# Kernel optimization log

Measured on AMD Instinct MI355X. Metric: run time of the kernel, lower is better.

Reference implementation:

```python
import jax, jax.numpy as jnp
import numpy as np

B, CIN, COUT, H, W, K, PAD, STRIDE = 32, 64, 64, 224, 224, 3, 1, 1


def setup_inputs() -> dict:
    key = jax.random.key(0)
    kx, kw, kb = jax.random.split(key, 3)
    x = jax.random.normal(kx, (B, CIN, H, W), dtype=jnp.float32)
    weight = jax.random.normal(kw, (COUT, CIN, K, K), dtype=jnp.float32)
    bias = jax.random.normal(kb, (COUT,), dtype=jnp.float32)
    return {"x": x, "weight": weight, "bias": bias}


def reference(x, weight, bias):
    # Binarize weights with sign (matches torch.sign: sign(0) == 0).
    w_bin = jnp.sign(weight)
    out = jax.lax.conv_general_dilated(
        x, w_bin,
        window_strides=(STRIDE, STRIDE),
        padding=[(PAD, PAD), (PAD, PAD)],
        dimension_numbers=("NCHW", "OIHW", "NCHW"),
    )
    return out + bias[None, :, None, None]
```

## Files before the change

### kernel.cpp

```cpp
#include <hip/hip_runtime.h>

#define BATCH 32
#define CIN_  64
#define COUT_ 64
#define H_    224
#define W_    224
#define HW_   (H_*W_)

#define HT     2
#define WTILE  112
#define XS_P   116
#define NROWS  (HT+2)
#define NTILES (WTILE/16)

typedef __bf16 bf16x4 __attribute__((ext_vector_type(4)));
typedef __bf16 bf16x8 __attribute__((ext_vector_type(8)));
typedef float  f32x4  __attribute__((ext_vector_type(4)));

__global__ void bc_prep(const float* __restrict__ w, __bf16* __restrict__ wp) {
    int gid = blockIdx.x * 256 + threadIdx.x;
    if (gid >= COUT_ * CIN_ * 9) return;
    int co  = gid / (CIN_ * 9);
    int rem = gid - co * (CIN_ * 9);
    int ci  = rem / 9;
    int t   = rem - ci * 9;
    float v = w[gid];
    float s = (v > 0.0f) ? 1.0f : ((v < 0.0f) ? -1.0f : 0.0f);
    wp[t * (COUT_ * CIN_) + co * CIN_ + ci] = (__bf16)s;
}

__global__ __launch_bounds__(256, 2)
void bc_main(const float* __restrict__ x, const __bf16* __restrict__ wp,
             const float* __restrict__ bias, float* __restrict__ out) {
    __shared__ __attribute__((aligned(16))) __bf16 xs[NROWS * XS_P * 64];

    const int htile = blockIdx.x;
    const int wt    = blockIdx.y;
    const int b     = blockIdx.z;
    const int h0 = htile * HT;
    const int w0 = wt * WTILE;

    const int tid  = threadIdx.x;
    const int lane = tid & 63;
    const int wave = tid >> 6;
    const int col  = lane & 15;
    const int quad = lane >> 4;

    bf16x8 afrag[18];
    {
        const int m = wave * 16 + col;
        #pragma unroll
        for (int kc = 0; kc < 18; ++kc) {
            const int tap = kc >> 1;
            const int cib = (kc & 1) * 32 + quad * 8;
            afrag[kc] = *(const bf16x8*)(wp + tap * (COUT_ * CIN_) + m * CIN_ + cib);
        }
    }
    float biasr[4];
    #pragma unroll
    for (int r = 0; r < 4; ++r) biasr[r] = bias[wave * 16 + quad * 4 + r];

    const int cig   = tid >> 4;
    const int ci0   = cig * 4;
    const int cc    = cig >> 1;
    const int chalf = (cig & 1) * 4;

    #pragma unroll
    for (int r = 0; r < NROWS; ++r) {
        const int hin = h0 - 1 + r;
        const bool rowok = (hin >= 0) && (hin < H_);
        const float* src = x + (size_t)b * CIN_ * HW_ + (size_t)hin * W_;
        #pragma unroll
        for (int s = 0; s < 2; ++s) {
            const int pxg = (tid & 15) + s * 16;
            const int wbase = w0 - 4 + pxg * 4;
            float vv[4][4];
            #pragma unroll
            for (int j = 0; j < 4; ++j) {
                const float* pr = src + (size_t)(ci0 + j) * HW_ + wbase;
                if (rowok && wbase >= 0 && wbase + 3 < W_) {
                    float4 f = *(const float4*)pr;
                    vv[j][0] = f.x; vv[j][1] = f.y; vv[j][2] = f.z; vv[j][3] = f.w;
                } else {
                    #pragma unroll
                    for (int i = 0; i < 4; ++i) {
                        const int wg = wbase + i;
                        vv[j][i] = (rowok && wg >= 0 && wg < W_) ? pr[i] : 0.0f;
                    }
                }
            }
            #pragma unroll
            for (int i = 0; i < 4; ++i) {
                const int p = pxg * 4 + i - 3;
                if (p >= 0 && p < XS_P) {
                    bf16x4 pk;
                    pk[0] = (__bf16)vv[0][i];
                    pk[1] = (__bf16)vv[1][i];
                    pk[2] = (__bf16)vv[2][i];
                    pk[3] = (__bf16)vv[3][i];
                    const int cp = cc ^ ((p >> 1) & 7);
                    *(bf16x4*)&xs[(r * XS_P + p) * 64 + cp * 8 + chalf] = pk;
                }
            }
        }
    }
    __syncthreads();

    #pragma unroll
    for (int hh = 0; hh < HT; ++hh) {
        for (int nt = 0; nt < NTILES; ++nt) {
            const int pw = nt * 16;
            const int pc = pw + col;
            f32x4 acc = (f32x4){0.f, 0.f, 0.f, 0.f};
            #pragma unroll
            for (int kc = 0; kc < 18; ++kc) {
                const int tap = kc >> 1;
                const int dh  = tap / 3;
                const int dw  = tap - dh * 3;
                const int pin = pc + dw;
                const int c   = (kc & 1) * 4 + quad;
                const int cp  = c ^ ((pin >> 1) & 7);
                const bf16x8* bsrc =
                    (const bf16x8*)&xs[((hh + dh) * XS_P + pin) * 64 + cp * 8];
                acc = __builtin_amdgcn_mfma_f32_16x16x32_bf16(afrag[kc], *bsrc, acc, 0, 0, 0);
            }
            float* op = out + (((size_t)b * COUT_ + wave * 16 + quad * 4) * H_ + (h0 + hh)) * W_
                            + (w0 + pw + col);
            #pragma unroll
            for (int r = 0; r < 4; ++r)
                op[(size_t)r * HW_] = acc[r] + biasr[r];
        }
    }
}

extern "C" void kernel_launch(void* const* d_in, const int* in_sizes, int n_in,
                              void* d_out, int out_size, void* d_ws, size_t ws_size,
                              hipStream_t stream) {
    const float* x    = (const float*)d_in[0];
    const float* w    = (const float*)d_in[1];
    const float* bias = (const float*)d_in[2];
    float* out = (float*)d_out;
    __bf16* wp = (__bf16*)d_ws;

    bc_prep<<<dim3((COUT_ * CIN_ * 9 + 255) / 256), dim3(256), 0, stream>>>(w, wp);
    bc_main<<<dim3(H_ / HT, W_ / WTILE, BATCH), dim3(256), 0, stream>>>(x, wp, bias, out);
}
```

Baseline: 918.6 us.

## Switch compute loop to 32x32x16 MFMA tiles covering two rows per wave

```diff
diff --git a/kernel.cpp b/kernel.cpp
--- a/kernel.cpp
+++ b/kernel.cpp
@@ -11,11 +11,12 @@
 #define WTILE  112
 #define XS_P   116
 #define NROWS  (HT+2)
-#define NTILES (WTILE/16)
+#define NG     7
 
 typedef __bf16 bf16x4 __attribute__((ext_vector_type(4)));
 typedef __bf16 bf16x8 __attribute__((ext_vector_type(8)));
 typedef float  f32x4  __attribute__((ext_vector_type(4)));
+typedef float  f32x16 __attribute__((ext_vector_type(16)));
 
 __global__ void bc_prep(const float* __restrict__ w, __bf16* __restrict__ wp) {
     int gid = blockIdx.x * 256 + threadIdx.x;
@@ -36,29 +37,32 @@
 
     const int htile = blockIdx.x;
     const int wt    = blockIdx.y;
-    const int b     = blockIdx.z;
+    const int bb    = blockIdx.z;
     const int h0 = htile * HT;
     const int w0 = wt * WTILE;
 
     const int tid  = threadIdx.x;
     const int lane = tid & 63;
     const int wave = tid >> 6;
-    const int col  = lane & 15;
-    const int quad = lane >> 4;
+    const int ct   = wave & 1;
+    const int gs   = wave >> 1;
+    const int col  = lane & 31;
+    const int kh   = lane >> 5;
 
-    bf16x8 afrag[18];
+    bf16x8 afrag[36];
     {
-        const int m = wave * 16 + col;
+        const int m = ct * 32 + col;
         #pragma unroll
-        for (int kc = 0; kc < 18; ++kc) {
-            const int tap = kc >> 1;
-            const int cib = (kc & 1) * 32 + quad * 8;
-            afrag[kc] = *(const bf16x8*)(wp + tap * (COUT_ * CIN_) + m * CIN_ + cib);
+        for (int s = 0; s < 36; ++s) {
+            const int tap = s >> 2;
+            const int cib = (s & 3) * 16 + kh * 8;
+            afrag[s] = *(const bf16x8*)(wp + tap * (COUT_ * CIN_) + m * CIN_ + cib);
         }
     }
-    float biasr[4];
+    float biasr[16];
     #pragma unroll
-    for (int r = 0; r < 4; ++r) biasr[r] = bias[wave * 16 + quad * 4 + r];
+    for (int r = 0; r < 16; ++r)
+        biasr[r] = bias[ct * 32 + 4 * kh + (r & 3) + 8 * (r >> 2)];
 
     const int cig   = tid >> 4;
     const int ci0   = cig * 4;
@@ -69,7 +73,7 @@
     for (int r = 0; r < NROWS; ++r) {
         const int hin = h0 - 1 + r;
         const bool rowok = (hin >= 0) && (hin < H_);
-        const float* src = x + (size_t)b * CIN_ * HW_ + (size_t)hin * W_;
+        const float* src = x + (size_t)bb * CIN_ * HW_ + (size_t)hin * W_;
         #pragma unroll
         for (int s = 0; s < 2; ++s) {
             const int pxg = (tid & 15) + s * 16;
@@ -106,29 +110,33 @@
     }
     __syncthreads();
 
-    #pragma unroll
-    for (int hh = 0; hh < HT; ++hh) {
-        for (int nt = 0; nt < NTILES; ++nt) {
-            const int pw = nt * 16;
-            const int pc = pw + col;
-            f32x4 acc = (f32x4){0.f, 0.f, 0.f, 0.f};
-            #pragma unroll
-            for (int kc = 0; kc < 18; ++kc) {
-                const int tap = kc >> 1;
-                const int dh  = tap / 3;
-                const int dw  = tap - dh * 3;
-                const int pin = pc + dw;
-                const int c   = (kc & 1) * 4 + quad;
-                const int cp  = c ^ ((pin >> 1) & 7);
-                const bf16x8* bsrc =
-                    (const bf16x8*)&xs[((hh + dh) * XS_P + pin) * 64 + cp * 8];
-                acc = __builtin_amdgcn_mfma_f32_16x16x32_bf16(afrag[kc], *bsrc, acc, 0, 0, 0);
-            }
-            float* op = out + (((size_t)b * COUT_ + wave * 16 + quad * 4) * H_ + (h0 + hh)) * W_
-                            + (w0 + pw + col);
-            #pragma unroll
-            for (int r = 0; r < 4; ++r)
-                op[(size_t)r * HW_] = acc[r] + biasr[r];
+    const int hh  = col >> 4;
+    const int pxl = col & 15;
+    const int swz0 = ((pxl + 0) >> 1) & 7;
+    const int swz1 = ((pxl + 1) >> 1) & 7;
+    const int swz2 = ((pxl + 2) >> 1) & 7;
+
+    for (int g = gs; g < NG; g += 2) {
+        f32x16 acc = {};
+        #pragma unroll
+        for (int s = 0; s < 36; ++s) {
+            const int tap = s >> 2;
+            const int dh  = tap / 3;
+            const int dw  = tap - dh * 3;
+            const int swz = (dw == 0) ? swz0 : ((dw == 1) ? swz1 : swz2);
+            const int c   = (s & 3) * 2 + kh;
+            const int cp  = c ^ swz;
+            const int pin = g * 16 + pxl + dw;
+            const bf16x8* bsrc =
+                (const bf16x8*)&xs[((hh + dh) * XS_P + pin) * 64 + cp * 8];
+            acc = __builtin_amdgcn_mfma_f32_32x32x16_bf16(afrag[s], *bsrc, acc, 0, 0, 0);
+        }
+        float* op = out + ((size_t)bb * COUT_ + ct * 32 + 4 * kh) * (size_t)HW_
+                        + (size_t)(h0 + hh) * W_ + (w0 + g * 16 + pxl);
+        #pragma unroll
+        for (int r = 0; r < 16; ++r) {
+            const int co_r = (r & 3) + 8 * (r >> 2);
+            op[(size_t)co_r * HW_] = acc[r] + biasr[r];
         }
     }
 }
```

Result: no change. 932.8 us (+1.5%).
